# Performance work log

Measured on AMD Instinct MI355X. Metric: run time of the kernel, lower is better.

Reference implementation:

```python
import jax, jax.numpy as jnp
import numpy as np

B, T, C = 2, 2048, 1024
N_HEAD, N_KV_HEAD, N_GLOBAL_HEAD = 16, 8, 8
HEAD_DIM = C // N_HEAD  # 64
Q_PER_KV = N_HEAD // N_KV_HEAD  # 2
N_GLOBAL_KV = N_GLOBAL_HEAD // Q_PER_KV  # 4
VE_GATE_CH = 32


def setup_inputs() -> dict:
    key = jax.random.key(0)
    ks = jax.random.split(key, 8)
    x = jax.random.normal(ks[0], (B, T, C), jnp.float32)
    ve = jax.random.normal(ks[1], (B, T, N_KV_HEAD * HEAD_DIM), jnp.float32)
    # rotary cos/sin: [T, 1, head_dim//2]
    half = HEAD_DIM // 2
    inv_freq = 1.0 / (10000.0 ** (np.arange(half, dtype=np.float32) / half))
    ang = np.arange(T, dtype=np.float32)[:, None] * inv_freq[None, :]
    cos = jnp.asarray(np.cos(ang))[:, None, :]
    sin = jnp.asarray(np.sin(ang))[:, None, :]
    s = 0.02
    Wq = jax.random.normal(ks[2], (C, N_HEAD * HEAD_DIM), jnp.float32) * s
    Wk = jax.random.normal(ks[3], (C, N_KV_HEAD * HEAD_DIM), jnp.float32) * s
    Wv = jax.random.normal(ks[4], (C, N_KV_HEAD * HEAD_DIM), jnp.float32) * s
    Wproj = jax.random.normal(ks[5], (C, C), jnp.float32) * s
    Wgate = jax.random.normal(ks[6], (VE_GATE_CH, N_KV_HEAD), jnp.float32) * s
    return {"x": x, "ve": ve, "cos": cos, "sin": sin, "Wq": Wq, "Wk": Wk,
            "Wv": Wv, "Wproj": Wproj, "Wgate": Wgate, "window": 512}


def _rope(x, cos, sin):
    # x: [B,T,H,D]; cos/sin: [T,1,D/2]
    d = x.shape[-1] // 2
    x1, x2 = x[..., :d], x[..., d:]
    return jnp.concatenate([x1 * cos + x2 * sin, -x1 * sin + x2 * cos], axis=-1)


def _rmsnorm(x):
    eps = jnp.finfo(x.dtype).eps
    return x * jax.lax.rsqrt(jnp.mean(x * x, axis=-1, keepdims=True) + eps)


def _attn(q, k, v, mask):
    # q,k,v: [B,T,H,D]; mask: [T,T] bool (True = allowed)
    scale = 1.0 / jnp.sqrt(jnp.asarray(q.shape[-1], q.dtype))
    scores = jnp.einsum('bqhd,bkhd->bhqk', q, k) * scale
    scores = jnp.where(mask[None, None], scores, jnp.finfo(scores.dtype).min)
    p = jax.nn.softmax(scores, axis=-1)
    return jnp.einsum('bhqk,bkhd->bqhd', p, v)


def reference(x, ve, cos, sin, Wq, Wk, Wv, Wproj, Wgate, window):
    q = (x @ Wq).reshape(B, T, N_HEAD, HEAD_DIM)
    k = (x @ Wk).reshape(B, T, N_KV_HEAD, HEAD_DIM)
    v = (x @ Wv).reshape(B, T, N_KV_HEAD, HEAD_DIM)
    # value-embedding gate
    gate = 2.0 * jax.nn.sigmoid(x[..., :VE_GATE_CH] @ Wgate)  # [B,T,n_kv]
    v = v + gate[..., None] * ve.reshape(B, T, N_KV_HEAD, HEAD_DIM)
    q, k = _rope(q, cos, sin), _rope(k, cos, sin)
    q, k = _rmsnorm(q), _rmsnorm(k)
    # split global / local heads
    qg, ql = q[:, :, :N_GLOBAL_HEAD], q[:, :, N_GLOBAL_HEAD:]
    kg, kl = k[:, :, :N_GLOBAL_KV], k[:, :, N_GLOBAL_KV:]
    vg, vl = v[:, :, :N_GLOBAL_KV], v[:, :, N_GLOBAL_KV:]
    # GQA: expand kv heads
    kg, vg = jnp.repeat(kg, Q_PER_KV, axis=2), jnp.repeat(vg, Q_PER_KV, axis=2)
    kl, vl = jnp.repeat(kl, Q_PER_KV, axis=2), jnp.repeat(vl, Q_PER_KV, axis=2)
    i = jnp.arange(T)[:, None]
    j = jnp.arange(T)[None, :]
    causal = j <= i
    local_mask = causal & (j >= i - window)  # flash window_size=(window, 0)
    yg = _attn(qg, kg, vg, causal)
    yl = _attn(ql, kl, vl, local_mask)
    y = jnp.concatenate([yg, yl], axis=2).reshape(B, T, C)
    return y @ Wproj
```

## Files before the change

kernel.cpp:

```cpp
#include <hip/hip_runtime.h>
#include <hip/hip_bf16.h>

#define BB 2
#define TT 2048
#define CC 1024
#define NH 16
#define NKV 8
#define HD 64

typedef __attribute__((ext_vector_type(8))) short short8;
typedef __attribute__((ext_vector_type(4))) float float4v;

__device__ __forceinline__ ushort f2bf(float f) {
    __hip_bfloat16 h = __float2bfloat16(f);
    union { __hip_bfloat16 h; ushort u; } v; v.h = h; return v.u;
}
__device__ __forceinline__ float bf2f(ushort u) {
    union { unsigned int i; float f; } v; v.i = ((unsigned int)u) << 16; return v.f;
}

__device__ __forceinline__ void gload16(const ushort* g, ushort* l) {
    __builtin_amdgcn_global_load_lds(
        (const __attribute__((address_space(1))) unsigned int*)g,
        (__attribute__((address_space(3))) unsigned int*)l, 16, 0, 0);
}

__device__ __forceinline__ void transpose_tile(
    const float* __restrict__ src, ushort* __restrict__ dst,
    int Kd, int Nd, int kt, int nt, float* tile )
{
    const int tid = threadIdx.x;
    {
        int r = tid >> 2, c = (tid & 3) * 16;
        #pragma unroll
        for (int i = 0; i < 4; i++) {
            float4 v = *(const float4*)&src[(size_t)(kt + r) * Nd + nt + c + i * 4];
            tile[r * 65 + c + i * 4 + 0] = v.x;
            tile[r * 65 + c + i * 4 + 1] = v.y;
            tile[r * 65 + c + i * 4 + 2] = v.z;
            tile[r * 65 + c + i * 4 + 3] = v.w;
        }
    }
    __syncthreads();
    {
        int n = tid >> 2, k = (tid & 3) * 16;
        #pragma unroll
        for (int i = 0; i < 2; i++) {
            ushort u[8];
            #pragma unroll
            for (int j = 0; j < 8; j++) u[j] = f2bf(tile[(k + i * 8 + j) * 65 + n]);
            *(uint4*)&dst[(size_t)(nt + n) * Kd + kt + k + i * 8] = *(uint4*)u;
        }
    }
}

__global__ __launch_bounds__(256) void prep_kernel(
    const float* __restrict__ x, ushort* __restrict__ xb,
    const float* __restrict__ Wq, const float* __restrict__ Wk,
    const float* __restrict__ Wv, const float* __restrict__ Wproj,
    ushort* __restrict__ WqkvT, ushort* __restrict__ WpT)
{
    __shared__ float tile[64 * 65];
    const int bid = blockIdx.x;
    if (bid < 4096) {
        int i = (bid * 256 + threadIdx.x) * 4;
        float4 v = *(const float4*)&x[i];
        xb[i + 0] = f2bf(v.x);
        xb[i + 1] = f2bf(v.y);
        xb[i + 2] = f2bf(v.z);
        xb[i + 3] = f2bf(v.w);
        return;
    }
    int t = bid - 4096;
    if (t < 256) {
        transpose_tile(Wq, WqkvT, 1024, 1024, (t >> 4) * 64, (t & 15) * 64, tile);
    } else if (t < 384) {
        t -= 256;
        transpose_tile(Wk, WqkvT + (size_t)1024 * 1024, 1024, 512, (t >> 3) * 64, (t & 7) * 64, tile);
    } else if (t < 512) {
        t -= 384;
        transpose_tile(Wv, WqkvT + (size_t)1536 * 1024, 1024, 512, (t >> 3) * 64, (t & 7) * 64, tile);
    } else {
        t -= 512;
        transpose_tile(Wproj, WpT, 1024, 1024, (t >> 4) * 64, (t & 15) * 64, tile);
    }
}

template<int BM, int OBF16>
__global__ __launch_bounds__(256) void gemm_bt_kernel(
    const ushort* __restrict__ A, const ushort* __restrict__ Bt,
    void* __restrict__ Cp, int M, int N, int K, int ldc)
{
    constexpr int RT = BM / 32;
    __shared__ ushort As[BM][32];
    __shared__ ushort Bs[128][32];

    const int m0 = blockIdx.x * BM;
    const int n0 = blockIdx.y * 128;
    const int tid = threadIdx.x;
    const int lane = tid & 63;
    const int w = tid >> 6;
    const int lr = lane & 15, lc = lane >> 4;
    const int wm = (w >> 1) * (BM / 2), wn = (w & 1) * 64;

    float4v acc[RT][4] = {};

    for (int k0 = 0; k0 < K; k0 += 32) {
        #pragma unroll
        for (int s = 0; s < BM / 64; s++) {
            int rb = w * (BM / 4) + s * 16;
            gload16(&A[(size_t)(m0 + rb + (lane >> 2)) * K + k0 + (lane & 3) * 8], &As[rb][0]);
        }
        #pragma unroll
        for (int s = 0; s < 2; s++) {
            int rb = w * 32 + s * 16;
            gload16(&Bt[(size_t)(n0 + rb + (lane >> 2)) * K + k0 + (lane & 3) * 8], &Bs[rb][0]);
        }
        __syncthreads();

        short8 af[RT], bf[4];
        #pragma unroll
        for (int t = 0; t < RT; t++)
            af[t] = *(const short8*)&As[wm + t * 16 + lr][lc * 8];
        #pragma unroll
        for (int t = 0; t < 4; t++)
            bf[t] = *(const short8*)&Bs[wn + t * 16 + lr][lc * 8];
        #pragma unroll
        for (int rt = 0; rt < RT; rt++)
            #pragma unroll
            for (int ct = 0; ct < 4; ct++)
                acc[rt][ct] = __builtin_amdgcn_mfma_f32_16x16x32_bf16(af[rt], bf[ct], acc[rt][ct], 0, 0, 0);
        __syncthreads();
    }

    #pragma unroll
    for (int rt = 0; rt < RT; rt++)
        #pragma unroll
        for (int ct = 0; ct < 4; ct++)
            #pragma unroll
            for (int r = 0; r < 4; r++) {
                int row = m0 + wm + rt * 16 + lc * 4 + r;
                int col = n0 + wn + ct * 16 + lr;
                if (OBF16) ((ushort*)Cp)[(size_t)row * ldc + col] = f2bf(acc[rt][ct][r]);
                else       ((float*)Cp)[(size_t)row * ldc + col] = acc[rt][ct][r];
            }
}

__global__ __launch_bounds__(256) void qkv_post_kernel(
    const ushort* __restrict__ qkv, const float* __restrict__ x,
    const float* __restrict__ ve, const float* __restrict__ cosb,
    const float* __restrict__ sinb, const float* __restrict__ wgate,
    ushort* __restrict__ Qb, ushort* __restrict__ Kb, ushort* __restrict__ Vn)
{
    const int bt = blockIdx.x;
    const int b = bt >> 11, t = bt & 2047;
    const int tid = threadIdx.x;
    const int lane = tid & 63;
    const int w = tid >> 6;
    __shared__ float gateS[8];

    {
        int g = tid >> 5, i = tid & 31;
        float p = x[(size_t)bt * CC + i] * wgate[i * 8 + g];
        #pragma unroll
        for (int off = 16; off; off >>= 1) p += __shfl_down(p, off, 32);
        if (i == 0) gateS[g] = 2.f / (1.f + __expf(-p));
    }
    __syncthreads();

    const float c = cosb[t * 32 + (lane & 31)];
    const float s = sinb[t * 32 + (lane & 31)];
    for (int hh = w; hh < 24; hh += 4) {
        const ushort* z = &qkv[(size_t)bt * 2048 + hh * 64];
        float v = bf2f(z[lane]);
        float other = __shfl_xor(v, 32);
        float x1 = (lane < 32) ? v : other;
        float x2 = (lane < 32) ? other : v;
        float val = (lane < 32) ? (x1 * c + x2 * s) : (-x1 * s + x2 * c);
        float ss = val * val;
        #pragma unroll
        for (int off = 32; off; off >>= 1) ss += __shfl_xor(ss, off);
        float scale = rsqrtf(ss * (1.f / 64.f) + 1.1920929e-07f);
        ushort ob = f2bf(val * scale);
        if (hh < 16) Qb[(((size_t)b * NH + hh) * TT + t) * HD + lane] = ob;
        else         Kb[(((size_t)b * NKV + (hh - 16)) * TT + t) * HD + lane] = ob;
    }

    for (int e = tid; e < NKV * HD; e += 256) {
        int kh = e >> 6, d = e & 63;
        float v = bf2f(qkv[(size_t)bt * 2048 + 1536 + e]) + gateS[kh] * ve[(size_t)bt * 512 + e];
        Vn[(((size_t)b * NKV + kh) * TT + t) * HD + d] = f2bf(v);
    }
}

__global__ __launch_bounds__(256) void v_transpose_kernel(
    const ushort* __restrict__ Vn, ushort* __restrict__ Vt)
{
    __shared__ ushort tile[64][72];
    const int t0 = blockIdx.x * 64;
    const int bh = blockIdx.y;
    const ushort* src = &Vn[(size_t)bh * TT * HD + (size_t)t0 * HD];
    ushort* dst = &Vt[(size_t)bh * HD * TT + t0];
    const int tid = threadIdx.x;
    {
        int r = tid >> 2, c = (tid & 3) * 16;
        #pragma unroll
        for (int i = 0; i < 2; i++)
            *(uint4*)&tile[r][c + i * 8] = *(const uint4*)&src[(size_t)r * HD + c + i * 8];
    }
    __syncthreads();
    {
        int d = tid >> 2, c = (tid & 3) * 16;
        #pragma unroll
        for (int i = 0; i < 2; i++) {
            ushort u[8];
            #pragma unroll
            for (int j = 0; j < 8; j++) u[j] = tile[c + i * 8 + j][d];
            *(uint4*)&dst[(size_t)d * TT + c + i * 8] = *(uint4*)u;
        }
    }
}

__global__ __launch_bounds__(256) void attn_kernel(
    const ushort* __restrict__ Qb, const ushort* __restrict__ Kb,
    const ushort* __restrict__ Vt, ushort* __restrict__ Yb,
    const int* __restrict__ winp)
{
    const int gid = blockIdx.x;
    int b, h, qw;
    if (gid < 1024) { qw = 63 - (gid >> 4); h = (gid >> 1) & 7; b = gid & 1; }
    else { int j = gid - 1024; qw = 63 - (j >> 4); h = 8 + ((j >> 1) & 7); b = j & 1; }

    const int q0 = qw * 32;
    const int kvh = h >> 1;
    const bool local = (h >= 8);
    int window = *winp;
    if (window < 0 || window > TT) window = TT;
    const int tid = threadIdx.x;
    const int w = tid >> 6;
    const int lane = tid & 63;
    const int lr = lane & 15, lc = lane >> 4;

    __shared__ ushort Ps[4][16][72];
    __shared__ float4v Ol[4][4][64];
    __shared__ float Ll[4][16];

    const ushort* qbase = &Qb[(((size_t)b * NH + h) * TT + q0) * HD];
    short8 qf[2][2];
    #pragma unroll
    for (int rt = 0; rt < 2; rt++)
        #pragma unroll
        for (int xh = 0; xh < 2; xh++)
            qf[rt][xh] = *(const short8*)&qbase[(size_t)(rt * 16 + lr) * HD + xh * 32 + lc * 8];

    float4v o[2][4] = {};
    float l_[2] = {0.f, 0.f};

    const ushort* Kbase = &Kb[((size_t)b * NKV + kvh) * TT * HD];
    const ushort* Vbase = &Vt[((size_t)b * NKV + kvh) * HD * TT];

    const int qlast = q0 + 31;
    int jstart = 0;
    if (local) { int js = q0 - window; if (js > 0) jstart = js & ~63; }
    const int j0first = jstart + w * 64;

    short8 kf[4][2];
    if (j0first <= qlast) {
        #pragma unroll
        for (int jt = 0; jt < 4; jt++) {
            const ushort* kp = &Kbase[(size_t)(j0first + jt * 16 + lr) * HD + lc * 8];
            kf[jt][0] = *(const short8*)kp;
            kf[jt][1] = *(const short8*)(kp + 32);
        }
    }

    for (int j0 = j0first; j0 <= qlast; j0 += 256) {
        short8 vf[4][2];
        #pragma unroll
        for (int ct = 0; ct < 4; ct++) {
            const ushort* vp = &Vbase[(size_t)(ct * 16 + lr) * TT + j0 + lc * 8];
            vf[ct][0] = *(const short8*)vp;
            vf[ct][1] = *(const short8*)(vp + 32);
        }
        short8 kn[4][2];
        const bool more = (j0 + 256 <= qlast);
        if (more) {
            #pragma unroll
            for (int jt = 0; jt < 4; jt++) {
                const ushort* kp = &Kbase[(size_t)(j0 + 256 + jt * 16 + lr) * HD + lc * 8];
                kn[jt][0] = *(const short8*)kp;
                kn[jt][1] = *(const short8*)(kp + 32);
            }
        }

        float4v st[2][4];
        #pragma unroll
        for (int jt = 0; jt < 4; jt++)
            #pragma unroll
            for (int rt = 0; rt < 2; rt++) {
                float4v z = {};
                z = __builtin_amdgcn_mfma_f32_16x16x32_bf16(kf[jt][0], qf[rt][0], z, 0, 0, 0);
                z = __builtin_amdgcn_mfma_f32_16x16x32_bf16(kf[jt][1], qf[rt][1], z, 0, 0, 0);
                st[rt][jt] = z;
            }

        const bool need_c = (j0 + 63 > q0);
        const bool need_w = local && (j0 < qlast - window);

        #pragma unroll
        for (int rt = 0; rt < 2; rt++) {
            const int qrow = q0 + rt * 16 + lr;
            float p[4][4];
            if (need_c || need_w) {
                #pragma unroll
                for (int jt = 0; jt < 4; jt++)
                    #pragma unroll
                    for (int r = 0; r < 4; r++) {
                        int key = j0 + jt * 16 + lc * 4 + r;
                        bool ok = (key <= qrow) && (!local || key >= qrow - window);
                        p[jt][r] = ok ? __expf(st[rt][jt][r] * 0.125f) : 0.f;
                    }
            } else {
                #pragma unroll
                for (int jt = 0; jt < 4; jt++)
                    #pragma unroll
                    for (int r = 0; r < 4; r++)
                        p[jt][r] = __expf(st[rt][jt][r] * 0.125f);
            }
            float s0 = (p[0][0] + p[0][1]) + (p[0][2] + p[0][3]);
            float s1 = (p[1][0] + p[1][1]) + (p[1][2] + p[1][3]);
            float s2 = (p[2][0] + p[2][1]) + (p[2][2] + p[2][3]);
            float s3 = (p[3][0] + p[3][1]) + (p[3][2] + p[3][3]);
            l_[rt] += (s0 + s1) + (s2 + s3);

            #pragma unroll
            for (int jt = 0; jt < 4; jt++) {
                ushort4 u;
                u.x = f2bf(p[jt][0]); u.y = f2bf(p[jt][1]);
                u.z = f2bf(p[jt][2]); u.w = f2bf(p[jt][3]);
                *(ushort4*)&Ps[w][lr][jt * 16 + lc * 4] = u;
            }
            short8 pb0 = *(const short8*)&Ps[w][lr][lc * 8];
            short8 pb1 = *(const short8*)&Ps[w][lr][32 + lc * 8];
            #pragma unroll
            for (int ct = 0; ct < 4; ct++) {
                o[rt][ct] = __builtin_amdgcn_mfma_f32_16x16x32_bf16(vf[ct][0], pb0, o[rt][ct], 0, 0, 0);
                o[rt][ct] = __builtin_amdgcn_mfma_f32_16x16x32_bf16(vf[ct][1], pb1, o[rt][ct], 0, 0, 0);
            }
        }

        if (more) {
            #pragma unroll
            for (int jt = 0; jt < 4; jt++) {
                kf[jt][0] = kn[jt][0];
                kf[jt][1] = kn[jt][1];
            }
        }
    }

    #pragma unroll
    for (int rt = 0; rt < 2; rt++) {
        l_[rt] += __shfl_xor(l_[rt], 16);
        l_[rt] += __shfl_xor(l_[rt], 32);
    }

    #pragma unroll
    for (int rt = 0; rt < 2; rt++) {
        #pragma unroll
        for (int ct = 0; ct < 4; ct++) Ol[w][ct][lane] = o[rt][ct];
        if (lc == 0) Ll[w][lr] = l_[rt];
        __syncthreads();

        {
            const int ct = w;
            float ltot = (Ll[0][lr] + Ll[1][lr]) + (Ll[2][lr] + Ll[3][lr]);
            float inv = 1.f / fmaxf(ltot, 1e-20f);
            float4v a0 = Ol[0][ct][lane], a1 = Ol[1][ct][lane];
            float4v a2 = Ol[2][ct][lane], a3 = Ol[3][ct][lane];
            int qrow = q0 + rt * 16 + lr;
            ushort4 u;
            u.x = f2bf(((a0[0] + a1[0]) + (a2[0] + a3[0])) * inv);
            u.y = f2bf(((a0[1] + a1[1]) + (a2[1] + a3[1])) * inv);
            u.z = f2bf(((a0[2] + a1[2]) + (a2[2] + a3[2])) * inv);
            u.w = f2bf(((a0[3] + a1[3]) + (a2[3] + a3[3])) * inv);
            *(ushort4*)&Yb[((size_t)b * TT + qrow) * CC + h * 64 + ct * 16 + lc * 4] = u;
        }
        if (rt == 0) __syncthreads();
    }
}

extern "C" void kernel_launch(void* const* d_in, const int* in_sizes, int n_in,
                              void* d_out, int out_size, void* d_ws, size_t ws_size,
                              hipStream_t stream) {
    (void)in_sizes; (void)n_in; (void)out_size; (void)ws_size;
    const float* x     = (const float*)d_in[0];
    const float* ve    = (const float*)d_in[1];
    const float* cosb  = (const float*)d_in[2];
    const float* sinb  = (const float*)d_in[3];
    const float* Wq    = (const float*)d_in[4];
    const float* Wk    = (const float*)d_in[5];
    const float* Wv    = (const float*)d_in[6];
    const float* Wproj = (const float*)d_in[7];
    const float* Wgate = (const float*)d_in[8];
    const int*   winp  = (const int*)d_in[9];
    float* out = (float*)d_out;

    char* ws = (char*)d_ws;
    ushort* qkvb  = (ushort*)ws;
    ushort* Yb    = (ushort*)ws;
    ushort* xb    = (ushort*)(ws + 33554432);
    ushort* Vnb   = (ushort*)(ws + 33554432);
    ushort* WqkvT = (ushort*)(ws + 41943040);
    ushort* WpT   = (ushort*)(ws + 46137344);
    ushort* Qb    = (ushort*)(ws + 48234496);
    ushort* Kb    = (ushort*)(ws + 56623104);
    ushort* Vtb   = (ushort*)(ws + 60817408);

    dim3 blk(256);
    prep_kernel<<<dim3(4864), blk, 0, stream>>>(x, xb, Wq, Wk, Wv, Wproj, WqkvT, WpT);
    gemm_bt_kernel<64, 1><<<dim3(64, 16), blk, 0, stream>>>(xb, WqkvT, qkvb, 4096, 2048, 1024, 2048);
    qkv_post_kernel<<<dim3(BB * TT), blk, 0, stream>>>(qkvb, x, ve, cosb, sinb, Wgate, Qb, Kb, Vnb);
    v_transpose_kernel<<<dim3(TT / 64, BB * NKV), blk, 0, stream>>>(Vnb, Vtb);
    attn_kernel<<<dim3(2048), blk, 0, stream>>>(Qb, Kb, Vtb, Yb, winp);
    gemm_bt_kernel<64, 0><<<dim3(64, 8), blk, 0, stream>>>(Yb, WpT, out, 4096, 1024, 1024, 1024);
}
```

Measured before the change: 221.4 us.

## Repack attention probabilities in registers via permlane swaps instead of LDS

Replaces the per-wave LDS round trip used to reshape softmax probabilities into the MFMA B-operand layout with packed bf16 conversions and v_permlane32/16_swap register shuffles. It also switches the exponential to a native exp2 with the scale folded into one constant, and adds a min-blocks-per-CU hint to launch_bounds. This removes LDS writes and reads plus their waits from the inner loop and frees the Ps shared buffer. The risks are a wrong permutation mapping for the operand layout and register pressure from the occupancy hint.

```diff
diff --git a/kernel.cpp b/kernel.cpp
--- a/kernel.cpp
+++ b/kernel.cpp
@@ -17,6 +17,14 @@
 }
 __device__ __forceinline__ float bf2f(ushort u) {
     union { unsigned int i; float f; } v; v.i = ((unsigned int)u) << 16; return v.f;
+}
+
+__device__ __forceinline__ float fexp2(float x) {
+#if __has_builtin(__builtin_amdgcn_exp2f)
+    return __builtin_amdgcn_exp2f(x);
+#else
+    return __expf(x * 0.69314718056f);
+#endif
 }
 
 __device__ __forceinline__ void gload16(const ushort* g, ushort* l) {
@@ -221,7 +229,7 @@
     }
 }
 
-__global__ __launch_bounds__(256) void attn_kernel(
+__global__ __launch_bounds__(256, 4) void attn_kernel(
     const ushort* __restrict__ Qb, const ushort* __restrict__ Kb,
     const ushort* __restrict__ Vt, ushort* __restrict__ Yb,
     const int* __restrict__ winp)
@@ -241,7 +249,6 @@
     const int lane = tid & 63;
     const int lr = lane & 15, lc = lane >> 4;
 
-    __shared__ ushort Ps[4][16][72];
     __shared__ float4v Ol[4][4][64];
     __shared__ float Ll[4][16];
 
@@ -263,6 +270,8 @@
     int jstart = 0;
     if (local) { int js = q0 - window; if (js > 0) jstart = js & ~63; }
     const int j0first = jstart + w * 64;
+
+    const float ESC = 0.1803368801f;
 
     short8 kf[4][2];
     if (j0first <= qlast) {
@@ -318,14 +327,14 @@
                     for (int r = 0; r < 4; r++) {
                         int key = j0 + jt * 16 + lc * 4 + r;
                         bool ok = (key <= qrow) && (!local || key >= qrow - window);
-                        p[jt][r] = ok ? __expf(st[rt][jt][r] * 0.125f) : 0.f;
+                        p[jt][r] = ok ? fexp2(st[rt][jt][r] * ESC) : 0.f;
                     }
             } else {
                 #pragma unroll
                 for (int jt = 0; jt < 4; jt++)
                     #pragma unroll
                     for (int r = 0; r < 4; r++)
-                        p[jt][r] = __expf(st[rt][jt][r] * 0.125f);
+                        p[jt][r] = fexp2(st[rt][jt][r] * ESC);
             }
             float s0 = (p[0][0] + p[0][1]) + (p[0][2] + p[0][3]);
             float s1 = (p[1][0] + p[1][1]) + (p[1][2] + p[1][3]);
@@ -333,19 +342,33 @@
             float s3 = (p[3][0] + p[3][1]) + (p[3][2] + p[3][3]);
             l_[rt] += (s0 + s1) + (s2 + s3);
 
+            unsigned int pk[4][2];
             #pragma unroll
             for (int jt = 0; jt < 4; jt++) {
-                ushort4 u;
-                u.x = f2bf(p[jt][0]); u.y = f2bf(p[jt][1]);
-                u.z = f2bf(p[jt][2]); u.w = f2bf(p[jt][3]);
-                *(ushort4*)&Ps[w][lr][jt * 16 + lc * 4] = u;
-            }
-            short8 pb0 = *(const short8*)&Ps[w][lr][lc * 8];
-            short8 pb1 = *(const short8*)&Ps[w][lr][32 + lc * 8];
+                asm("v_cvt_pk_bf16_f32 %0, %1, %2"
+                    : "=v"(pk[jt][0]) : "v"(p[jt][0]), "v"(p[jt][1]));
+                asm("v_cvt_pk_bf16_f32 %0, %1, %2"
+                    : "=v"(pk[jt][1]) : "v"(p[jt][2]), "v"(p[jt][3]));
+            }
+            asm("v_permlane32_swap_b32 %0, %1" : "+v"(pk[0][0]), "+v"(pk[1][0]));
+            asm("v_permlane16_swap_b32 %0, %1" : "+v"(pk[0][0]), "+v"(pk[1][0]));
+            asm("v_permlane32_swap_b32 %0, %1" : "+v"(pk[0][1]), "+v"(pk[1][1]));
+            asm("v_permlane16_swap_b32 %0, %1" : "+v"(pk[0][1]), "+v"(pk[1][1]));
+            asm("v_permlane32_swap_b32 %0, %1" : "+v"(pk[2][0]), "+v"(pk[3][0]));
+            asm("v_permlane16_swap_b32 %0, %1" : "+v"(pk[2][0]), "+v"(pk[3][0]));
+            asm("v_permlane32_swap_b32 %0, %1" : "+v"(pk[2][1]), "+v"(pk[3][1]));
+            asm("v_permlane16_swap_b32 %0, %1" : "+v"(pk[2][1]), "+v"(pk[3][1]));
+
+            union { unsigned int u[4]; short8 s; } P0, P1;
+            P0.u[0] = pk[0][0]; P0.u[1] = pk[0][1];
+            P0.u[2] = pk[1][0]; P0.u[3] = pk[1][1];
+            P1.u[0] = pk[2][0]; P1.u[1] = pk[2][1];
+            P1.u[2] = pk[3][0]; P1.u[3] = pk[3][1];
+
             #pragma unroll
             for (int ct = 0; ct < 4; ct++) {
-                o[rt][ct] = __builtin_amdgcn_mfma_f32_16x16x32_bf16(vf[ct][0], pb0, o[rt][ct], 0, 0, 0);
-                o[rt][ct] = __builtin_amdgcn_mfma_f32_16x16x32_bf16(vf[ct][1], pb1, o[rt][ct], 0, 0, 0);
+                o[rt][ct] = __builtin_amdgcn_mfma_f32_16x16x32_bf16(vf[ct][0], P0.s, o[rt][ct], 0, 0, 0);
+                o[rt][ct] = __builtin_amdgcn_mfma_f32_16x16x32_bf16(vf[ct][1], P1.s, o[rt][ct], 0, 0, 0);
             }
         }
 
```

Measured after the change: 325.8 us. +47.2%, slower.
